# Kernel optimization log

Hardware: AMD Instinct MI355X
Metric: run time of the kernel (lower is better)

The kernel has to match this reference:

```python
import jax, jax.numpy as jnp
import numpy as np

B, C, L, D = 8, 256, 2048, 128  # batch, in_channels, seq_len, n_factor


def setup_inputs() -> dict:
    key = jax.random.key(0)
    ks = jax.random.split(key, 8)
    s = 1.0 / np.sqrt(C)
    return {
        "x_inner": jax.random.normal(ks[0], (B, C, L), jnp.float32),
        "x_outer": jax.random.normal(ks[1], (B, C, L), jnp.float32),
        "Wq": jax.random.normal(ks[2], (D, C), jnp.float32) * s,
        "bq": jax.random.normal(ks[3], (D,), jnp.float32) * 0.01,
        "Wk": jax.random.normal(ks[4], (D, C), jnp.float32) * s,
        "bk": jax.random.normal(ks[5], (D,), jnp.float32) * 0.01,
        "Wv": jax.random.normal(ks[6], (D, C), jnp.float32) * s,
        "bv": jax.random.normal(ks[7], (D,), jnp.float32) * 0.01,
    }


def reference(x_inner, x_outer, Wq, bq, Wk, bk, Wv, bv):
    # kernel-size-1 Conv1d == per-position linear over channels; permute -> [B, L, D]
    q = jnp.einsum('bcl,dc->bld', x_inner, Wq) + bq  # [B, Lq, D]
    k = jnp.einsum('bcl,dc->bld', x_outer, Wk) + bk  # [B, Lk, D]
    v = jnp.einsum('bcl,dc->bld', x_outer, Wv) + bv  # [B, Lk, D]
    scores = jnp.einsum('bqd,bkd->bqk', q, k) / jnp.sqrt(jnp.asarray(D, q.dtype))
    attn = jax.nn.softmax(scores, axis=2)            # [B, Lq, Lk]
    return jnp.einsum('bqk,bkd->bqd', attn, v)       # [B, Lq, D]
```

## Files before the change

kernel.cpp:

```cpp
#include <hip/hip_runtime.h>
#include <hip/hip_bf16.h>

#define NB 8
#define NC 256
#define NL 2048
#define ND 128
#define NROWS (NB * NL)
#define QKV_ELEMS ((size_t)NB * NL * ND)
#define W_ELEMS (ND * NC)
#define XS_STRIDE 264

typedef __attribute__((ext_vector_type(8))) short bf16x8;
typedef __attribute__((ext_vector_type(4))) float f32x4;
typedef __attribute__((ext_vector_type(16))) float f32x16;

__device__ __forceinline__ unsigned short f2bf(float f) {
    union { float f; unsigned u; } v; v.f = f;
    unsigned r = v.u + 0x7fffu + ((v.u >> 16) & 1u);
    return (unsigned short)(r >> 16);
}

__device__ __forceinline__ void load_lds16(const unsigned short* g, unsigned short* l) {
    __builtin_amdgcn_global_load_lds((const __attribute__((address_space(1))) unsigned int*)g,
                                     (__attribute__((address_space(3))) unsigned int*)l, 16, 0, 0);
}

__global__ void cast_w3(const float* __restrict__ wq, const float* __restrict__ wk,
                        const float* __restrict__ wv, unsigned short* __restrict__ dst) {
    int i = blockIdx.x * blockDim.x + threadIdx.x;
    if (i >= 3 * W_ELEMS) return;
    int sel = i / W_ELEMS, off = i - sel * W_ELEMS;
    const float* s = (sel == 0) ? wq : (sel == 1) ? wk : wv;
    dst[i] = f2bf(s[off]);
}

__global__ __launch_bounds__(256, 4) void proj_direct(const float* __restrict__ xi,
                                                      const float* __restrict__ xo,
                                                      const unsigned short* __restrict__ Wall,
                                                      const float* __restrict__ bq,
                                                      const float* __restrict__ bk,
                                                      const float* __restrict__ bv,
                                                      unsigned short* __restrict__ Qb,
                                                      unsigned short* __restrict__ Kb,
                                                      unsigned short* __restrict__ Vtb) {
    __shared__ unsigned short xs[64 * XS_STRIDE];
    int b = blockIdx.x >> 5, lt = blockIdx.x & 31, l0 = lt * 64;
    int y = blockIdx.y;
    int wave = threadIdx.x >> 6, lane = threadIdx.x & 63;
    int ln = lane & 15, quad = lane >> 4;

    const float* xsrc = (y == 0 ? xi : xo) + (size_t)b * NC * NL + l0;
    int l4 = (lane & 15) * 4;
    int cr0 = wave * 4 + (lane >> 4);
    #pragma unroll
    for (int g = 0; g < 4; g++) {
        float4 r[4];
        #pragma unroll
        for (int gi = 0; gi < 4; gi++) {
            int c = cr0 + (g * 4 + gi) * 16;
            r[gi] = *reinterpret_cast<const float4*>(xsrc + (size_t)c * NL + l4);
        }
        #pragma unroll
        for (int gi = 0; gi < 4; gi++) {
            int c = cr0 + (g * 4 + gi) * 16;
            xs[(l4 + 0) * XS_STRIDE + c] = f2bf(r[gi].x);
            xs[(l4 + 1) * XS_STRIDE + c] = f2bf(r[gi].y);
            xs[(l4 + 2) * XS_STRIDE + c] = f2bf(r[gi].z);
            xs[(l4 + 3) * XS_STRIDE + c] = f2bf(r[gi].w);
        }
    }
    __syncthreads();

    {
        const unsigned short* Wb = Wall + (size_t)y * W_ELEMS;
        const float* bias = y ? bk : bq;
        unsigned short* out = y ? Kb : Qb;
        int m0w = wave * 16;
        f32x4 acc[8] = {};
        #pragma unroll
        for (int s = 0; s < 8; s++) {
            bf16x8 af = *reinterpret_cast<const bf16x8*>(xs + (m0w + ln) * XS_STRIDE + s * 32 + quad * 8);
            #pragma unroll
            for (int t = 0; t < 8; t++) {
                bf16x8 bfr = *reinterpret_cast<const bf16x8*>(Wb + (size_t)(t * 16 + ln) * NC + s * 32 + quad * 8);
                acc[t] = __builtin_amdgcn_mfma_f32_16x16x32_bf16(af, bfr, acc[t], 0, 0, 0);
            }
        }
        #pragma unroll
        for (int t = 0; t < 8; t++) {
            int col = t * 16 + ln;
            float bi = bias[col];
            #pragma unroll
            for (int r = 0; r < 4; r++)
                out[(size_t)(b * NL + l0 + m0w + quad * 4 + r) * ND + col] = f2bf(acc[t][r] + bi);
        }
    }
    if (y == 1) {
        const unsigned short* Wb = Wall + 2 * (size_t)W_ELEMS;
        f32x4 acc[2][4] = {};
        #pragma unroll
        for (int s = 0; s < 8; s++) {
            bf16x8 wf0 = *reinterpret_cast<const bf16x8*>(Wb + (size_t)(wave * 32 + ln) * NC + s * 32 + quad * 8);
            bf16x8 wf1 = *reinterpret_cast<const bf16x8*>(Wb + (size_t)(wave * 32 + 16 + ln) * NC + s * 32 + quad * 8);
            #pragma unroll
            for (int t = 0; t < 4; t++) {
                bf16x8 xb = *reinterpret_cast<const bf16x8*>(xs + (t * 16 + ln) * XS_STRIDE + s * 32 + quad * 8);
                acc[0][t] = __builtin_amdgcn_mfma_f32_16x16x32_bf16(wf0, xb, acc[0][t], 0, 0, 0);
                acc[1][t] = __builtin_amdgcn_mfma_f32_16x16x32_bf16(wf1, xb, acc[1][t], 0, 0, 0);
            }
        }
        #pragma unroll
        for (int u = 0; u < 2; u++)
            #pragma unroll
            for (int t = 0; t < 4; t++)
                #pragma unroll
                for (int r = 0; r < 4; r++) {
                    int d = wave * 32 + u * 16 + quad * 4 + r;
                    Vtb[(size_t)(b * ND + d) * NL + l0 + t * 16 + ln] = f2bf(acc[u][t][r] + bv[d]);
                }
    }
}

__global__ __launch_bounds__(256, 2) void flash_attn_split(const unsigned short* __restrict__ Q,
                                                           const unsigned short* __restrict__ K,
                                                           const unsigned short* __restrict__ Vt,
                                                           float* __restrict__ Opart,
                                                           float* __restrict__ lbuf,
                                                           int kvlen) {
    __shared__ unsigned short kbuf[64 * 128];
    __shared__ unsigned short vbuf[128 * 64];
    __shared__ unsigned short pbuf[4][32 * 64];
    int b = blockIdx.x >> 4, qt = blockIdx.x & 15;
    int sp = blockIdx.y;
    int kv0 = sp * kvlen;
    int wave = threadIdx.x >> 6, lane = threadIdx.x & 63;
    int l31 = lane & 31, h = lane >> 5;
    int m0 = qt * 128 + wave * 32;
    const float scale = 0.08838834764831845f * 1.4426950408889634f;

    bf16x8 qf[8];
    const unsigned short* qrow = Q + (size_t)(b * NL + m0 + l31) * ND + h * 8;
    #pragma unroll
    for (int s = 0; s < 8; s++) qf[s] = *reinterpret_cast<const bf16x8*>(qrow + s * 16);

    float lsum = 0.f;
    f32x16 o_acc[4] = {};

    unsigned short* pw = pbuf[wave];
    const unsigned short* kg = K + (size_t)b * NL * ND;
    const unsigned short* vg = Vt + (size_t)b * ND * NL;

    int krt = wave * 16 + (lane >> 4);
    int kjs_lane = lane & 15;
    int vdt = wave * 32 + (lane >> 3);
    int vjs_lane = lane & 7;

    for (int kt = kv0; kt < kv0 + kvlen; kt += 64) {
        #pragma unroll
        for (int i = 0; i < 4; i++) {
            int rt = krt + i * 4;
            int js = kjs_lane ^ (rt & 15);
            load_lds16(kg + (size_t)(kt + rt) * ND + js * 8, kbuf + (wave * 16 + i * 4) * 128);
        }
        #pragma unroll
        for (int i = 0; i < 4; i++) {
            int dt = vdt + i * 8;
            int js = vjs_lane ^ (dt & 7);
            load_lds16(vg + (size_t)dt * NL + kt + js * 8, vbuf + (wave * 32 + i * 8) * 64);
        }
        __syncthreads();

        f32x16 sacc[2] = {};
        #pragma unroll
        for (int tt = 0; tt < 2; tt++) {
            const unsigned short* krow_p = kbuf + (tt * 32 + l31) * 128;
            #pragma unroll
            for (int s = 0; s < 8; s++) {
                bf16x8 kf = *reinterpret_cast<const bf16x8*>(krow_p + (((s * 2 + h) ^ (lane & 15)) << 3));
                sacc[tt] = __builtin_amdgcn_mfma_f32_32x32x16_bf16(kf, qf[s], sacc[tt], 0, 0, 0);
            }
        }
        #pragma unroll
        for (int tt = 0; tt < 2; tt++) {
            #pragma unroll
            for (int g = 0; g < 4; g++) {
                float p0 = __builtin_exp2f(sacc[tt][g * 4 + 0] * scale);
                float p1 = __builtin_exp2f(sacc[tt][g * 4 + 1] * scale);
                float p2 = __builtin_exp2f(sacc[tt][g * 4 + 2] * scale);
                float p3 = __builtin_exp2f(sacc[tt][g * 4 + 3] * scale);
                lsum += (p0 + p1) + (p2 + p3);
                ushort4 o4 = { f2bf(p0), f2bf(p1), f2bf(p2), f2bf(p3) };
                int chunk = tt * 4 + g;
                *reinterpret_cast<ushort4*>(pw + l31 * 64 + ((chunk ^ (l31 & 7)) << 3) + h * 4) = o4;
            }
        }
        bf16x8 pb[4];
        #pragma unroll
        for (int step = 0; step < 4; step++)
            pb[step] = *reinterpret_cast<const bf16x8*>(pw + l31 * 64 + (((step * 2 + h) ^ (l31 & 7)) << 3));
        #pragma unroll
        for (int dt = 0; dt < 4; dt++) {
            const unsigned short* vrow = vbuf + (dt * 32 + l31) * 64;
            #pragma unroll
            for (int step = 0; step < 4; step++) {
                bf16x8 vf = *reinterpret_cast<const bf16x8*>(vrow + (((step * 2 + h) ^ (l31 & 7)) << 3));
                o_acc[dt] = __builtin_amdgcn_mfma_f32_32x32x16_bf16(vf, pb[step], o_acc[dt], 0, 0, 0);
            }
        }
        __syncthreads();
    }
    lsum += __shfl_xor(lsum, 32);

    float* op = Opart + (size_t)sp * QKV_ELEMS;
    int qrow_g = b * NL + m0 + l31;
    if (lane < 32) lbuf[(size_t)sp * NROWS + qrow_g] = lsum;
    #pragma unroll
    for (int dt = 0; dt < 4; dt++) {
        #pragma unroll
        for (int g = 0; g < 4; g++) {
            f32x4 v4 = { o_acc[dt][g * 4 + 0], o_acc[dt][g * 4 + 1],
                         o_acc[dt][g * 4 + 2], o_acc[dt][g * 4 + 3] };
            *reinterpret_cast<f32x4*>(op + (size_t)qrow_g * ND + dt * 32 + g * 8 + h * 4) = v4;
        }
    }
}

__global__ __launch_bounds__(256) void attn_merge(const float* __restrict__ Opart,
                                                  const float* __restrict__ lbuf,
                                                  float* __restrict__ out, int S) {
    int idx = blockIdx.x * 256 + threadIdx.x;
    int row = idx >> 5;
    int dg = (idx & 31) * 4;
    float L = 0.f;
    float4 acc = make_float4(0.f, 0.f, 0.f, 0.f);
    for (int s = 0; s < S; s++) {
        L += lbuf[(size_t)s * NROWS + row];
        float4 o = *reinterpret_cast<const float4*>(Opart + (size_t)s * QKV_ELEMS + (size_t)row * ND + dg);
        acc.x += o.x; acc.y += o.y; acc.z += o.z; acc.w += o.w;
    }
    float inv = 1.0f / L;
    float4 res = make_float4(acc.x * inv, acc.y * inv, acc.z * inv, acc.w * inv);
    *reinterpret_cast<float4*>(out + (size_t)row * ND + dg) = res;
}

extern "C" void kernel_launch(void* const* d_in, const int* in_sizes, int n_in,
                              void* d_out, int out_size, void* d_ws, size_t ws_size,
                              hipStream_t stream) {
    const float* x_inner = (const float*)d_in[0];
    const float* x_outer = (const float*)d_in[1];
    const float* Wq = (const float*)d_in[2];
    const float* bq = (const float*)d_in[3];
    const float* Wk = (const float*)d_in[4];
    const float* bk = (const float*)d_in[5];
    const float* Wv = (const float*)d_in[6];
    const float* bv = (const float*)d_in[7];
    float* out = (float*)d_out;

    size_t need4 = 34078720u + 3 * QKV_ELEMS * 2 + 3 * W_ELEMS * 2;
    int S = (ws_size >= need4) ? 4 : 2;
    size_t union_bytes = (S == 4) ? 34078720u : 17039360u;

    char* w = (char*)d_ws;
    float* Opart = (float*)w;
    float* lbuf = (float*)(w + (size_t)S * QKV_ELEMS * 4);
    unsigned short* Qb = (unsigned short*)(w + union_bytes);
    unsigned short* Kb = Qb + QKV_ELEMS;
    unsigned short* Vtb = Kb + QKV_ELEMS;
    unsigned short* Wall = Vtb + QKV_ELEMS;

    cast_w3<<<(3 * W_ELEMS + 255) / 256, 256, 0, stream>>>(Wq, Wk, Wv, Wall);
    dim3 pgrid(NB * (NL / 64), 2);
    proj_direct<<<pgrid, 256, 0, stream>>>(x_inner, x_outer, Wall, bq, bk, bv, Qb, Kb, Vtb);
    dim3 fgrid(NB * (NL / 128), S);
    flash_attn_split<<<fgrid, 256, 0, stream>>>(Qb, Kb, Vtb, Opart, lbuf, NL / S);
    attn_merge<<<(NROWS * ND / 4 + 255) / 256, 256, 0, stream>>>(Opart, lbuf, out, S);
}
```

Measured before the change: 152.2 us.

## Double-buffer K/V tiles in flash attention and split V projection into own blocks

After: 148.4 us. -2.5%, faster.

```diff
diff --git a/kernel.cpp b/kernel.cpp
--- a/kernel.cpp
+++ b/kernel.cpp
@@ -71,7 +71,7 @@
     }
     __syncthreads();
 
-    {
+    if (y < 2) {
         const unsigned short* Wb = Wall + (size_t)y * W_ELEMS;
         const float* bias = y ? bk : bq;
         unsigned short* out = y ? Kb : Qb;
@@ -94,8 +94,7 @@
             for (int r = 0; r < 4; r++)
                 out[(size_t)(b * NL + l0 + m0w + quad * 4 + r) * ND + col] = f2bf(acc[t][r] + bi);
         }
-    }
-    if (y == 1) {
+    } else {
         const unsigned short* Wb = Wall + 2 * (size_t)W_ELEMS;
         f32x4 acc[2][4] = {};
         #pragma unroll
@@ -127,8 +126,8 @@
                                                            float* __restrict__ Opart,
                                                            float* __restrict__ lbuf,
                                                            int kvlen) {
-    __shared__ unsigned short kbuf[64 * 128];
-    __shared__ unsigned short vbuf[128 * 64];
+    __shared__ unsigned short kbuf[2][64 * 128];
+    __shared__ unsigned short vbuf[2][128 * 64];
     __shared__ unsigned short pbuf[4][32 * 64];
     int b = blockIdx.x >> 4, qt = blockIdx.x & 15;
     int sp = blockIdx.y;
@@ -151,29 +150,50 @@
     const unsigned short* vg = Vt + (size_t)b * ND * NL;
 
     int krt = wave * 16 + (lane >> 4);
-    int kjs_lane = lane & 15;
+    int kjs = (lane & 15);
     int vdt = wave * 32 + (lane >> 3);
-    int vjs_lane = lane & 7;
-
-    for (int kt = kv0; kt < kv0 + kvlen; kt += 64) {
+    int vjs = (lane & 7);
+
+    {
+        int kt = kv0;
         #pragma unroll
         for (int i = 0; i < 4; i++) {
             int rt = krt + i * 4;
-            int js = kjs_lane ^ (rt & 15);
-            load_lds16(kg + (size_t)(kt + rt) * ND + js * 8, kbuf + (wave * 16 + i * 4) * 128);
+            load_lds16(kg + (size_t)(kt + rt) * ND + (kjs ^ (rt & 15)) * 8, kbuf[0] + (wave * 16 + i * 4) * 128);
         }
         #pragma unroll
         for (int i = 0; i < 4; i++) {
             int dt = vdt + i * 8;
-            int js = vjs_lane ^ (dt & 7);
-            load_lds16(vg + (size_t)dt * NL + kt + js * 8, vbuf + (wave * 32 + i * 8) * 64);
-        }
+            load_lds16(vg + (size_t)dt * NL + kt + (vjs ^ (dt & 7)) * 8, vbuf[0] + (wave * 32 + i * 8) * 64);
+        }
+    }
+
+    int niter = kvlen >> 6;
+    for (int it = 0; it < niter; it++) {
+        int cur = it & 1;
         __syncthreads();
 
+        if (it + 1 < niter) {
+            int kt = kv0 + (it + 1) * 64;
+            int nxt = cur ^ 1;
+            #pragma unroll
+            for (int i = 0; i < 4; i++) {
+                int rt = krt + i * 4;
+                load_lds16(kg + (size_t)(kt + rt) * ND + (kjs ^ (rt & 15)) * 8, kbuf[nxt] + (wave * 16 + i * 4) * 128);
+            }
+            #pragma unroll
+            for (int i = 0; i < 4; i++) {
+                int dt = vdt + i * 8;
+                load_lds16(vg + (size_t)dt * NL + kt + (vjs ^ (dt & 7)) * 8, vbuf[nxt] + (wave * 32 + i * 8) * 64);
+            }
+        }
+        const unsigned short* kb = kbuf[cur];
+        const unsigned short* vb = vbuf[cur];
+
         f32x16 sacc[2] = {};
         #pragma unroll
         for (int tt = 0; tt < 2; tt++) {
-            const unsigned short* krow_p = kbuf + (tt * 32 + l31) * 128;
+            const unsigned short* krow_p = kb + (tt * 32 + l31) * 128;
             #pragma unroll
             for (int s = 0; s < 8; s++) {
                 bf16x8 kf = *reinterpret_cast<const bf16x8*>(krow_p + (((s * 2 + h) ^ (lane & 15)) << 3));
@@ -200,14 +220,13 @@
             pb[step] = *reinterpret_cast<const bf16x8*>(pw + l31 * 64 + (((step * 2 + h) ^ (l31 & 7)) << 3));
         #pragma unroll
         for (int dt = 0; dt < 4; dt++) {
-            const unsigned short* vrow = vbuf + (dt * 32 + l31) * 64;
+            const unsigned short* vrow = vb + (dt * 32 + l31) * 64;
             #pragma unroll
             for (int step = 0; step < 4; step++) {
                 bf16x8 vf = *reinterpret_cast<const bf16x8*>(vrow + (((step * 2 + h) ^ (l31 & 7)) << 3));
                 o_acc[dt] = __builtin_amdgcn_mfma_f32_32x32x16_bf16(vf, pb[step], o_acc[dt], 0, 0, 0);
             }
         }
-        __syncthreads();
     }
     lsum += __shfl_xor(lsum, 32);
 
@@ -269,7 +288,7 @@
     unsigned short* Wall = Vtb + QKV_ELEMS;
 
     cast_w3<<<(3 * W_ELEMS + 255) / 256, 256, 0, stream>>>(Wq, Wk, Wv, Wall);
-    dim3 pgrid(NB * (NL / 64), 2);
+    dim3 pgrid(NB * (NL / 64), 3);
     proj_direct<<<pgrid, 256, 0, stream>>>(x_inner, x_outer, Wall, bq, bk, bv, Qb, Kb, Vtb);
     dim3 fgrid(NB * (NL / 128), S);
     flash_attn_split<<<fgrid, 256, 0, stream>>>(Qb, Kb, Vtb, Opart, lbuf, NL / S);
```
